# Performance work log

Hardware: AMD Instinct MI355X
Metric: run time of the kernel (lower is better)

## Reference

```python
import jax, jax.numpy as jnp
import numpy as np

B, L, E = 8, 2048, 128


def setup_inputs() -> dict:
    key = jax.random.key(0)
    k1, k2, k3, k4 = jax.random.split(key, 4)
    return {
        "Uq": jax.random.normal(k1, (B, L, E), dtype=jnp.float32),
        "Uid": jax.random.normal(k2, (B, L, E), dtype=jnp.float32),
        "mask": jnp.ones((L, L), dtype=jnp.float32),
        "Wc_w": jax.random.normal(k3, (3 * E,), dtype=jnp.float32) * 0.05,
        "Wc_b": jax.random.normal(k4, (), dtype=jnp.float32) * 0.05,
    }


def reference(Uq, Uid, mask, Wc_w, Wc_b):
    # Wc(cat(Uid, Uq, Uid*Uq)) decomposed into three direct projections —
    # exact same math as the Linear over the concatenation, never
    # materializing the [B, L, L, 3E] tensor.
    e = Uq.shape[-1]
    w_id, w_q, w_mul = Wc_w[:e], Wc_w[e:2 * e], Wc_w[2 * e:]
    s_id = jnp.einsum("bie,e->bi", Uid, w_id)          # [B, Lid]
    s_q = jnp.einsum("bje,e->bj", Uq, w_q)             # [B, Lq]
    s_mul = jnp.einsum("bie,bje,e->bij", Uid, Uq, w_mul)  # [B, Lid, Lq]
    S = (s_id[:, :, None] + s_q[:, None, :] + s_mul + Wc_b) * mask
    # S_D2Q = Softmax(dim=0) over the per-example [Lid, Lq] matrix -> axis=1
    P = jax.nn.softmax(S, axis=1)                      # [B, Lid, Lq]
    A_D2Q = jnp.einsum("bij,bje->bie", P, Uq)          # [B, Lid, E]
    M = jnp.einsum("bij,bkj->bik", P, P)               # P @ P^T, [B, Lid, Lid]
    A_Q2D = jnp.einsum("bik,bke->bie", M, Uid)         # [B, Lid, E]
    Vid = jnp.concatenate([Uid, A_D2Q, Uid * A_D2Q, Uid * A_Q2D], axis=-1)
    return Vid  # [B, Lid, 4E]
```

## Files before the change

kernel.cpp:

```cpp
#include <hip/hip_runtime.h>

#define L 2048
#define E 128
#define NB 8

typedef float f32x4 __attribute__((ext_vector_type(4)));
typedef short short8 __attribute__((ext_vector_type(8)));
typedef unsigned int u32;

static __device__ inline float bf2f(ushort u) {
  union { float f; u32 i; } v; v.i = ((u32)u) << 16; return v.f;
}
static __device__ inline ushort f2bf(float f) {
  union { float f; u32 i; } v; v.f = f;
  u32 x = v.i;
  return (ushort)((x + 0x7fffu + ((x >> 16) & 1u)) >> 16);
}

__device__ inline void glds16(const ushort* g, ushort* l) {
  __builtin_amdgcn_global_load_lds(
      (const __attribute__((address_space(1))) u32*)(const void*)g,
      (__attribute__((address_space(3))) u32*)(void*)l, 16, 0, 0);
}

__global__ __launch_bounds__(128) void k_prep(const float* __restrict__ Uq,
                                              const float* __restrict__ Uid,
                                              const float* __restrict__ Wcw,
                                              ushort* __restrict__ UqB,
                                              ushort* __restrict__ UidB,
                                              ushort* __restrict__ Uidw,
                                              float* __restrict__ s_id,
                                              float* __restrict__ s_q) {
  int r = blockIdx.x;
  int e = threadIdx.x;
  ushort uqu  = f2bf(Uq[(long)r * E + e]);
  ushort uidu = f2bf(Uid[(long)r * E + e]);
  float uqf = bf2f(uqu), uidf = bf2f(uidu);
  float wid  = bf2f(f2bf(Wcw[e]));
  float wq   = bf2f(f2bf(Wcw[E + e]));
  float wmul = bf2f(f2bf(Wcw[2 * E + e]));
  UqB[(long)r * E + e]  = uqu;
  UidB[(long)r * E + e] = uidu;
  Uidw[(long)r * E + e] = f2bf(uidf * wmul);
  float sid = uidf * wid, sq = uqf * wq;
  #pragma unroll
  for (int off = 32; off >= 1; off >>= 1) {
    sid += __shfl_down(sid, off, 64);
    sq  += __shfl_down(sq,  off, 64);
  }
  __shared__ float red[4];
  int wv = threadIdx.x >> 6;
  if ((threadIdx.x & 63) == 0) { red[wv * 2] = sid; red[wv * 2 + 1] = sq; }
  __syncthreads();
  if (threadIdx.x == 0) { s_id[r] = red[0] + red[2]; s_q[r] = red[1] + red[3]; }
}

__global__ __launch_bounds__(256) void k_maskT(const float* __restrict__ mask,
                                               ushort* __restrict__ maskT) {
  __shared__ ushort tile[32][33];
  int j0 = blockIdx.x * 32, i0 = blockIdx.y * 32;
  int tx = threadIdx.x, ty = threadIdx.y;
  #pragma unroll
  for (int r = ty; r < 32; r += 8)
    tile[r][tx] = f2bf(mask[(long)(i0 + r) * L + j0 + tx]);
  __syncthreads();
  #pragma unroll
  for (int r = ty; r < 32; r += 8)
    maskT[(long)(j0 + r) * L + i0 + tx] = tile[tx][r];
}

__global__ __launch_bounds__(256) void k_tr2(const ushort* __restrict__ s1,
                                             ushort* __restrict__ d1,
                                             const ushort* __restrict__ s2,
                                             ushort* __restrict__ d2) {
  __shared__ ushort tile[32][33];
  int zz = blockIdx.z;
  long base = (long)(zz & (NB - 1)) * L * E;
  const ushort* src = ((zz < NB) ? s1 : s2) + base;
  ushort* dst = ((zz < NB) ? d1 : d2) + base;
  int c0 = blockIdx.x * 32, r0 = blockIdx.y * 32;
  int tx = threadIdx.x, ty = threadIdx.y;
  #pragma unroll
  for (int i = ty; i < 32; i += 8)
    tile[i][tx] = src[(long)(r0 + i) * E + c0 + tx];
  __syncthreads();
  #pragma unroll
  for (int i = ty; i < 32; i += 8)
    dst[(long)(c0 + i) * L + r0 + tx] = tile[tx][i];
}

__device__ inline void gemm128_loop(const ushort* __restrict__ A,
                                    const ushort* __restrict__ B,
                                    long ldA, long ldB, int K,
                                    f32x4 acc[4][4],
                                    ushort* ldsA, ushort* ldsB) {
  const int t = threadIdx.x;
  const int w = t >> 6, lane = t & 63;
  const int mrow = lane & 15, quad = lane >> 4;
  const int lr = lane >> 3;
  const int lc = ((lane & 7) ^ lr) * 8;
  const int mh = (w & 1) * 64, nh = (w >> 1) * 64;
  for (int k0 = 0; k0 < K; k0 += 64) {
    __syncthreads();
    #pragma unroll
    for (int s = 0; s < 4; s++) {
      int row = w * 32 + s * 8 + lr;
      glds16(&A[(long)row * ldA + k0 + lc], &ldsA[w * 2048 + s * 512]);
      glds16(&B[(long)row * ldB + k0 + lc], &ldsB[w * 2048 + s * 512]);
    }
    __syncthreads();
    #pragma unroll
    for (int kk = 0; kk < 2; kk++) {
      short8 av[4], bv[4];
      #pragma unroll
      for (int mi = 0; mi < 4; mi++)
        av[mi] = *(const short8*)&ldsA[(mh + mi * 16 + mrow) * 64 +
                                       ((kk * 32 + quad * 8) ^ ((mrow & 7) << 3))];
      #pragma unroll
      for (int ni = 0; ni < 4; ni++)
        bv[ni] = *(const short8*)&ldsB[(nh + ni * 16 + mrow) * 64 +
                                       ((kk * 32 + quad * 8) ^ ((mrow & 7) << 3))];
      #pragma unroll
      for (int mi = 0; mi < 4; mi++)
        #pragma unroll
        for (int ni = 0; ni < 4; ni++)
          acc[mi][ni] = __builtin_amdgcn_mfma_f32_16x16x32_bf16(av[mi], bv[ni], acc[mi][ni], 0, 0, 0);
    }
  }
}

__device__ inline void gemm64x128_loop(const ushort* __restrict__ A,
                                       const ushort* __restrict__ B,
                                       long ldA, long ldB, int K,
                                       f32x4 acc[2][4],
                                       ushort* ldsA, ushort* ldsB) {
  const int t = threadIdx.x;
  const int w = t >> 6, lane = t & 63;
  const int mrow = lane & 15, quad = lane >> 4;
  const int lr = lane >> 3;
  const int lc = ((lane & 7) ^ lr) * 8;
  const int mh = (w & 1) * 32, nh = (w >> 1) * 64;
  for (int k0 = 0; k0 < K; k0 += 64) {
    __syncthreads();
    #pragma unroll
    for (int s = 0; s < 2; s++) {
      int row = w * 16 + s * 8 + lr;
      glds16(&A[(long)row * ldA + k0 + lc], &ldsA[w * 1024 + s * 512]);
    }
    #pragma unroll
    for (int s = 0; s < 4; s++) {
      int row = w * 32 + s * 8 + lr;
      glds16(&B[(long)row * ldB + k0 + lc], &ldsB[w * 2048 + s * 512]);
    }
    __syncthreads();
    #pragma unroll
    for (int kk = 0; kk < 2; kk++) {
      short8 av[2], bv[4];
      #pragma unroll
      for (int mi = 0; mi < 2; mi++)
        av[mi] = *(const short8*)&ldsA[(mh + mi * 16 + mrow) * 64 +
                                       ((kk * 32 + quad * 8) ^ ((mrow & 7) << 3))];
      #pragma unroll
      for (int ni = 0; ni < 4; ni++)
        bv[ni] = *(const short8*)&ldsB[(nh + ni * 16 + mrow) * 64 +
                                       ((kk * 32 + quad * 8) ^ ((mrow & 7) << 3))];
      #pragma unroll
      for (int mi = 0; mi < 2; mi++)
        #pragma unroll
        for (int ni = 0; ni < 4; ni++)
          acc[mi][ni] = __builtin_amdgcn_mfma_f32_16x16x32_bf16(av[mi], bv[ni], acc[mi][ni], 0, 0, 0);
    }
  }
}

__global__ __launch_bounds__(256) void k_scores(const ushort* __restrict__ Uq,
                                                const ushort* __restrict__ Uidw,
                                                const float* __restrict__ s_id,
                                                const float* __restrict__ s_q,
                                                const float* __restrict__ Wcb,
                                                const ushort* __restrict__ maskT,
                                                ushort* __restrict__ St,
                                                float* __restrict__ pm,
                                                float* __restrict__ ps, int b0) {
  __shared__ ushort lds[16384];
  ushort* ldsA = lds;
  ushort* ldsB = lds + 8192;
  int bz = blockIdx.z, b = b0 + bz;
  int m0 = blockIdx.x * 128;
  int n0 = blockIdx.y * 128;
  int tile_i = blockIdx.y;
  const ushort* A = Uq   + (long)b * L * E + (long)m0 * E;
  const ushort* B = Uidw + (long)b * L * E + (long)n0 * E;
  f32x4 acc[4][4] = {};
  gemm128_loop(A, B, E, E, E, acc, ldsA, ldsB);
  float bias = bf2f(f2bf(Wcb[0]));
  const int t = threadIdx.x, w = t >> 6, lane = t & 63;
  const int col = lane & 15, quad = lane >> 4;
  const int mh = (w & 1) * 64, nh = (w >> 1) * 64;

  __syncthreads();
  float sidv[4];
  #pragma unroll
  for (int ni = 0; ni < 4; ni++)
    sidv[ni] = s_id[b * L + n0 + nh + ni * 16 + col];
  #pragma unroll
  for (int mi = 0; mi < 4; mi++) {
    float sqv[4];
    #pragma unroll
    for (int rg = 0; rg < 4; rg++)
      sqv[rg] = s_q[b * L + m0 + mh + mi * 16 + quad * 4 + rg];
    #pragma unroll
    for (int ni = 0; ni < 4; ni++) {
      int cl = nh + ni * 16 + col;
      #pragma unroll
      for (int rg = 0; rg < 4; rg++) {
        int row = mh + mi * 16 + quad * 4 + rg;
        float v = acc[mi][ni][rg] + sqv[rg] + sidv[ni] + bias;
        lds[row * 128 + (cl ^ ((row & 7) << 3))] = f2bf(v);
      }
    }
  }
  __syncthreads();
  #pragma unroll
  for (int p = 0; p < 8; p++) {
    int r2 = p * 16 + (t >> 4);
    int cu = (t & 15) * 8;
    uint4 sv = *(const uint4*)&lds[r2 * 128 + (cu ^ ((r2 & 7) << 3))];
    int jg = m0 + r2;
    uint4 mv = *(const uint4*)&maskT[(long)jg * L + n0 + cu];
    ushort o[8]; float vv[8];
    const ushort* sp = (const ushort*)&sv;
    const ushort* mp = (const ushort*)&mv;
    #pragma unroll
    for (int k = 0; k < 8; k++) {
      o[k] = f2bf(bf2f(sp[k]) * bf2f(mp[k]));
      vv[k] = bf2f(o[k]);
    }
    *(uint4*)&St[(long)bz * L * L + (long)jg * L + n0 + cu] = *(const uint4*)&o[0];
    float lmx = vv[0];
    #pragma unroll
    for (int k = 1; k < 8; k++) lmx = fmaxf(lmx, vv[k]);
    #pragma unroll
    for (int off = 8; off >= 1; off >>= 1) lmx = fmaxf(lmx, __shfl_xor(lmx, off, 64));
    float lsum = 0.f;
    #pragma unroll
    for (int k = 0; k < 8; k++) lsum += __expf(vv[k] - lmx);
    #pragma unroll
    for (int off = 8; off >= 1; off >>= 1) lsum += __shfl_xor(lsum, off, 64);
    if ((t & 15) == 0) {
      long si = ((long)bz * L + jg) * 16 + tile_i;
      pm[si] = lmx; ps[si] = lsum;
    }
  }
}

__global__ __launch_bounds__(256) void k_sm_apply(ushort* __restrict__ St,
                                                  ushort* __restrict__ P,
                                                  const float* __restrict__ pm,
                                                  const float* __restrict__ ps) {
  __shared__ ushort tl[4 * 1056];
  __shared__ float smM[32], smI[32];
  int bz = blockIdx.y;
  int t = threadIdx.x, wid = t >> 6, lane = t & 63;
  int flat = blockIdx.x * 4 + wid;
  int j0 = (flat >> 6) * 32;
  int i0 = (flat & 63) * 32;
  if (t < 32) {
    const float* pmr = pm + ((long)bz * L + j0 + t) * 16;
    const float* psr = ps + ((long)bz * L + j0 + t) * 16;
    float m = pmr[0];
    #pragma unroll
    for (int k = 1; k < 16; k++) m = fmaxf(m, pmr[k]);
    float s = 0.f;
    #pragma unroll
    for (int k = 0; k < 16; k++) s += psr[k] * __expf(pmr[k] - m);
    smM[t] = m; smI[t] = 1.0f / s;
  }
  __syncthreads();
  ushort* Sb = St + (long)bz * L * L;
  ushort* Pb = P  + (long)bz * L * L;
  ushort* wt = tl + wid * 1056;
  int r = lane >> 1, c0 = (lane & 1) * 16;
  float m   = smM[r];
  float inv = smI[r];
  ushort* src = Sb + (long)(j0 + r) * L + i0 + c0;
  uint4 q0 = *(const uint4*)src;
  uint4 q1 = *(const uint4*)(src + 8);
  ushort o[16];
  const ushort* pr = (const ushort*)&q0;
  #pragma unroll
  for (int k = 0; k < 8; k++) o[k] = f2bf(__expf(bf2f(pr[k]) - m) * inv);
  pr = (const ushort*)&q1;
  #pragma unroll
  for (int k = 0; k < 8; k++) o[8 + k] = f2bf(__expf(bf2f(pr[k]) - m) * inv);
  *(uint4*)src       = *(const uint4*)&o[0];
  *(uint4*)(src + 8) = *(const uint4*)&o[8];
  #pragma unroll
  for (int k = 0; k < 16; k++) wt[(c0 + k) * 33 + r] = o[k];
  asm volatile("s_waitcnt lgkmcnt(0)" ::: "memory");
  __builtin_amdgcn_sched_barrier(0);
  ushort po[16];
  #pragma unroll
  for (int k = 0; k < 16; k++) po[k] = wt[r * 33 + c0 + k];
  ushort* pd = Pb + (long)(i0 + r) * L + j0 + c0;
  *(uint4*)pd       = *(const uint4*)&po[0];
  *(uint4*)(pd + 8) = *(const uint4*)&po[8];
}

__global__ __launch_bounds__(256) void k_gemm_Tt(const ushort* __restrict__ UidT,
                                                 const ushort* __restrict__ Pt,
                                                 ushort* __restrict__ Tt, int b0) {
  __shared__ ushort lds[12288];
  ushort* ldsA = lds;
  ushort* ldsB = lds + 4096;
  int bz = blockIdx.z, b = b0 + bz;
  int e0 = (blockIdx.x & 1) * 64;
  int j0 = (blockIdx.x >> 1) * 128;
  const ushort* A = UidT + (long)b * E * L + (long)e0 * L;
  const ushort* B = Pt   + (long)bz * L * L + (long)j0 * L;
  f32x4 acc[2][4] = {};
  gemm64x128_loop(A, B, L, L, L, acc, ldsA, ldsB);
  const int t = threadIdx.x, w = t >> 6, lane = t & 63;
  const int col = lane & 15, quad = lane >> 4;
  const int mh = (w & 1) * 32, nh = (w >> 1) * 64;
  __syncthreads();
  #pragma unroll
  for (int mi = 0; mi < 2; mi++)
    #pragma unroll
    for (int ni = 0; ni < 4; ni++) {
      int cl = nh + ni * 16 + col;
      #pragma unroll
      for (int rg = 0; rg < 4; rg++) {
        int row = mh + mi * 16 + quad * 4 + rg;
        lds[row * 128 + (cl ^ ((row & 7) << 3))] = f2bf(acc[mi][ni][rg]);
      }
    }
  __syncthreads();
  #pragma unroll
  for (int p = 0; p < 4; p++) {
    int r2 = p * 16 + (t >> 4);
    int cu = (t & 15) * 8;
    uint4 v = *(const uint4*)&lds[r2 * 128 + (cu ^ ((r2 & 7) << 3))];
    *(uint4*)&Tt[(long)b * E * L + (long)(e0 + r2) * L + j0 + cu] = v;
  }
}

__global__ __launch_bounds__(256) void k_gemm_A(const ushort* __restrict__ P,
                                                const ushort* __restrict__ UqT,
                                                const ushort* __restrict__ Tt,
                                                const ushort* __restrict__ UidB,
                                                float* __restrict__ out, int b0) {
  __shared__ ushort ldsA[64 * 64];
  __shared__ ushort ldsB[128 * 64];
  int bz = blockIdx.z, b = b0 + bz;
  int m0 = blockIdx.x * 64;
  int n0 = blockIdx.y * 128;
  const ushort* A = P + (long)bz * L * L + (long)m0 * L;
  const ushort* B = (blockIdx.y == 0) ? (UqT + (long)b * E * L)
                                      : (Tt  + (long)b * E * L);
  f32x4 acc[2][4] = {};
  gemm64x128_loop(A, B, L, L, L, acc, ldsA, ldsB);
  const int t = threadIdx.x, w = t >> 6, lane = t & 63;
  const int col = lane & 15, quad = lane >> 4;
  const int mh = (w & 1) * 32, nh = (w >> 1) * 64;
  #pragma unroll
  for (int mi = 0; mi < 2; mi++)
    #pragma unroll
    for (int ni = 0; ni < 4; ni++)
      #pragma unroll
      for (int rg = 0; rg < 4; rg++) {
        int ig = m0 + mh + mi * 16 + quad * 4 + rg;
        int c  = n0 + nh + ni * 16 + col;
        float a = acc[mi][ni][rg];
        float uidf = bf2f(UidB[(long)b * L * E + (long)ig * E + (c & 127)]);
        long ob = ((long)b * L + ig) * 512;
        if (c < 128) {
          out[ob + c]       = uidf;
          out[ob + 128 + c] = a;
          out[ob + 256 + c] = uidf * a;
        } else {
          out[ob + 256 + c] = uidf * a;
        }
      }
}

extern "C" void kernel_launch(void* const* d_in, const int* in_sizes, int n_in,
                              void* d_out, int out_size, void* d_ws, size_t ws_size,
                              hipStream_t stream) {
  const float* Uq   = (const float*)d_in[0];
  const float* Uid  = (const float*)d_in[1];
  const float* mask = (const float*)d_in[2];
  const float* Wcw  = (const float*)d_in[3];
  const float* Wcb  = (const float*)d_in[4];
  float* out = (float*)d_out;

  char* ws = (char*)d_ws;
  size_t off = 0;
  auto alloc = [&](size_t bytes) -> void* {
    void* p = ws + off; off += (bytes + 255) & ~(size_t)255; return p;
  };
  const size_t nUb = (size_t)NB * L * E * 2;
  ushort* UqB   = (ushort*)alloc(nUb);
  ushort* UidB  = (ushort*)alloc(nUb);
  ushort* Uidw  = (ushort*)alloc(nUb);
  ushort* UqT   = (ushort*)alloc(nUb);
  ushort* UidT  = (ushort*)alloc(nUb);
  ushort* Tt    = (ushort*)alloc(nUb);
  ushort* maskT = (ushort*)alloc((size_t)L * L * 2);
  float*  s_id  = (float*)alloc((size_t)NB * L * 4);
  float*  s_q   = (float*)alloc((size_t)NB * L * 4);
  float*  pm    = (float*)alloc((size_t)NB * L * 16 * 4);
  float*  ps    = (float*)alloc((size_t)NB * L * 16 * 4);
  const size_t per_batch = (size_t)L * L * 2;
  size_t avail = (ws_size > off + 2 * per_batch) ? (ws_size - off) : 2 * per_batch;
  int nb_c = (int)(avail / (2 * per_batch));
  if (nb_c < 1) nb_c = 1;
  if (nb_c > NB) nb_c = NB;
  ushort* St = (ushort*)(ws + off);
  ushort* P  = (ushort*)(ws + off + nb_c * per_batch);

  dim3 tb(32, 8);
  k_prep<<<NB * L, E, 0, stream>>>(Uq, Uid, Wcw, UqB, UidB, Uidw, s_id, s_q);
  k_maskT<<<dim3(L / 32, L / 32), tb, 0, stream>>>(mask, maskT);
  k_tr2<<<dim3(E / 32, L / 32, 2 * NB), tb, 0, stream>>>(UqB, UqT, UidB, UidT);

  for (int b0 = 0; b0 < NB; b0 += nb_c) {
    int nb = (NB - b0 < nb_c) ? (NB - b0) : nb_c;
    k_scores<<<dim3(L / 128, L / 128, nb), 256, 0, stream>>>(UqB, Uidw, s_id, s_q, Wcb, maskT, St, pm, ps, b0);
    k_sm_apply<<<dim3((L / 32) * (L / 32) / 4, nb), 256, 0, stream>>>(St, P, pm, ps);
    k_gemm_Tt<<<dim3(2 * (L / 128), 1, nb), 256, 0, stream>>>(UidT, St, Tt, b0);
    k_gemm_A<<<dim3(L / 64, 2, nb), 256, 0, stream>>>(P, UqT, Tt, UidB, out, b0);
  }
}
```

Baseline: 233.9 us.

## Drop softmax max-subtraction and defer normalization into GEMM epilogue

Scores kernel now writes exp(S) directly and emits only per-tile partial sums, removing the running max. A small kernel reduces the sums to a reciprocal per row. The transpose kernel only scales and transposes, no longer writing St back. The Tt GEMM consumes unnormalized exponentials and applies the reciprocal in its epilogue. This saves a full L×L read-modify-write pass and the exp work in the apply kernel, but risks overflow for large-magnitude scores because the max subtraction is gone.

```diff
diff --git a/kernel.cpp b/kernel.cpp
--- a/kernel.cpp
+++ b/kernel.cpp
@@ -180,7 +180,6 @@
                                                 const float* __restrict__ Wcb,
                                                 const ushort* __restrict__ maskT,
                                                 ushort* __restrict__ St,
-                                                float* __restrict__ pm,
                                                 float* __restrict__ ps, int b0) {
   __shared__ ushort lds[16384];
   ushort* ldsA = lds;
@@ -228,73 +227,59 @@
     uint4 sv = *(const uint4*)&lds[r2 * 128 + (cu ^ ((r2 & 7) << 3))];
     int jg = m0 + r2;
     uint4 mv = *(const uint4*)&maskT[(long)jg * L + n0 + cu];
-    ushort o[8]; float vv[8];
+    ushort o[8];
+    float lsum = 0.f;
     const ushort* sp = (const ushort*)&sv;
     const ushort* mp = (const ushort*)&mv;
     #pragma unroll
     for (int k = 0; k < 8; k++) {
-      o[k] = f2bf(bf2f(sp[k]) * bf2f(mp[k]));
-      vv[k] = bf2f(o[k]);
+      float ev = __expf(bf2f(sp[k]) * bf2f(mp[k]));
+      o[k] = f2bf(ev);
+      lsum += bf2f(o[k]);
     }
     *(uint4*)&St[(long)bz * L * L + (long)jg * L + n0 + cu] = *(const uint4*)&o[0];
-    float lmx = vv[0];
-    #pragma unroll
-    for (int k = 1; k < 8; k++) lmx = fmaxf(lmx, vv[k]);
-    #pragma unroll
-    for (int off = 8; off >= 1; off >>= 1) lmx = fmaxf(lmx, __shfl_xor(lmx, off, 64));
-    float lsum = 0.f;
-    #pragma unroll
-    for (int k = 0; k < 8; k++) lsum += __expf(vv[k] - lmx);
     #pragma unroll
     for (int off = 8; off >= 1; off >>= 1) lsum += __shfl_xor(lsum, off, 64);
     if ((t & 15) == 0) {
-      long si = ((long)bz * L + jg) * 16 + tile_i;
-      pm[si] = lmx; ps[si] = lsum;
-    }
-  }
-}
-
-__global__ __launch_bounds__(256) void k_sm_apply(ushort* __restrict__ St,
-                                                  ushort* __restrict__ P,
-                                                  const float* __restrict__ pm,
-                                                  const float* __restrict__ ps) {
+      ps[((long)bz * L + jg) * 16 + tile_i] = lsum;
+    }
+  }
+}
+
+__global__ __launch_bounds__(256) void k_redstats(const float* __restrict__ ps,
+                                                  float* __restrict__ lg) {
+  int idx = blockIdx.x * 256 + threadIdx.x;
+  const float* psr = ps + (long)idx * 16;
+  float s = 0.f;
+  #pragma unroll
+  for (int k = 0; k < 16; k++) s += psr[k];
+  lg[idx] = 1.0f / s;
+}
+
+__global__ __launch_bounds__(256) void k_ptr(const ushort* __restrict__ St,
+                                             ushort* __restrict__ P,
+                                             const float* __restrict__ lg) {
   __shared__ ushort tl[4 * 1056];
-  __shared__ float smM[32], smI[32];
   int bz = blockIdx.y;
   int t = threadIdx.x, wid = t >> 6, lane = t & 63;
   int flat = blockIdx.x * 4 + wid;
   int j0 = (flat >> 6) * 32;
   int i0 = (flat & 63) * 32;
-  if (t < 32) {
-    const float* pmr = pm + ((long)bz * L + j0 + t) * 16;
-    const float* psr = ps + ((long)bz * L + j0 + t) * 16;
-    float m = pmr[0];
-    #pragma unroll
-    for (int k = 1; k < 16; k++) m = fmaxf(m, pmr[k]);
-    float s = 0.f;
-    #pragma unroll
-    for (int k = 0; k < 16; k++) s += psr[k] * __expf(pmr[k] - m);
-    smM[t] = m; smI[t] = 1.0f / s;
-  }
-  __syncthreads();
-  ushort* Sb = St + (long)bz * L * L;
+  const ushort* Sb = St + (long)bz * L * L;
   ushort* Pb = P  + (long)bz * L * L;
   ushort* wt = tl + wid * 1056;
   int r = lane >> 1, c0 = (lane & 1) * 16;
-  float m   = smM[r];
-  float inv = smI[r];
-  ushort* src = Sb + (long)(j0 + r) * L + i0 + c0;
+  float inv = lg[bz * L + j0 + r];
+  const ushort* src = Sb + (long)(j0 + r) * L + i0 + c0;
   uint4 q0 = *(const uint4*)src;
   uint4 q1 = *(const uint4*)(src + 8);
   ushort o[16];
   const ushort* pr = (const ushort*)&q0;
   #pragma unroll
-  for (int k = 0; k < 8; k++) o[k] = f2bf(__expf(bf2f(pr[k]) - m) * inv);
+  for (int k = 0; k < 8; k++) o[k] = f2bf(bf2f(pr[k]) * inv);
   pr = (const ushort*)&q1;
   #pragma unroll
-  for (int k = 0; k < 8; k++) o[8 + k] = f2bf(__expf(bf2f(pr[k]) - m) * inv);
-  *(uint4*)src       = *(const uint4*)&o[0];
-  *(uint4*)(src + 8) = *(const uint4*)&o[8];
+  for (int k = 0; k < 8; k++) o[8 + k] = f2bf(bf2f(pr[k]) * inv);
   #pragma unroll
   for (int k = 0; k < 16; k++) wt[(c0 + k) * 33 + r] = o[k];
   asm volatile("s_waitcnt lgkmcnt(0)" ::: "memory");
@@ -308,7 +293,8 @@
 }
 
 __global__ __launch_bounds__(256) void k_gemm_Tt(const ushort* __restrict__ UidT,
-                                                 const ushort* __restrict__ Pt,
+                                                 const ushort* __restrict__ Et,
+                                                 const float* __restrict__ lg,
                                                  ushort* __restrict__ Tt, int b0) {
   __shared__ ushort lds[12288];
   ushort* ldsA = lds;
@@ -317,7 +303,7 @@
   int e0 = (blockIdx.x & 1) * 64;
   int j0 = (blockIdx.x >> 1) * 128;
   const ushort* A = UidT + (long)b * E * L + (long)e0 * L;
-  const ushort* B = Pt   + (long)bz * L * L + (long)j0 * L;
+  const ushort* B = Et   + (long)bz * L * L + (long)j0 * L;
   f32x4 acc[2][4] = {};
   gemm64x128_loop(A, B, L, L, L, acc, ldsA, ldsB);
   const int t = threadIdx.x, w = t >> 6, lane = t & 63;
@@ -329,10 +315,11 @@
     #pragma unroll
     for (int ni = 0; ni < 4; ni++) {
       int cl = nh + ni * 16 + col;
+      float sc = lg[(long)bz * L + j0 + cl];
       #pragma unroll
       for (int rg = 0; rg < 4; rg++) {
         int row = mh + mi * 16 + quad * 4 + rg;
-        lds[row * 128 + (cl ^ ((row & 7) << 3))] = f2bf(acc[mi][ni][rg]);
+        lds[row * 128 + (cl ^ ((row & 7) << 3))] = f2bf(acc[mi][ni][rg] * sc);
       }
     }
   __syncthreads();
@@ -409,7 +396,7 @@
   ushort* maskT = (ushort*)alloc((size_t)L * L * 2);
   float*  s_id  = (float*)alloc((size_t)NB * L * 4);
   float*  s_q   = (float*)alloc((size_t)NB * L * 4);
-  float*  pm    = (float*)alloc((size_t)NB * L * 16 * 4);
+  float*  lg    = (float*)alloc((size_t)NB * L * 4);
   float*  ps    = (float*)alloc((size_t)NB * L * 16 * 4);
   const size_t per_batch = (size_t)L * L * 2;
   size_t avail = (ws_size > off + 2 * per_batch) ? (ws_size - off) : 2 * per_batch;
@@ -426,9 +413,10 @@
 
   for (int b0 = 0; b0 < NB; b0 += nb_c) {
     int nb = (NB - b0 < nb_c) ? (NB - b0) : nb_c;
-    k_scores<<<dim3(L / 128, L / 128, nb), 256, 0, stream>>>(UqB, Uidw, s_id, s_q, Wcb, maskT, St, pm, ps, b0);
-    k_sm_apply<<<dim3((L / 32) * (L / 32) / 4, nb), 256, 0, stream>>>(St, P, pm, ps);
-    k_gemm_Tt<<<dim3(2 * (L / 128), 1, nb), 256, 0, stream>>>(UidT, St, Tt, b0);
+    k_scores<<<dim3(L / 128, L / 128, nb), 256, 0, stream>>>(UqB, Uidw, s_id, s_q, Wcb, maskT, St, ps, b0);
+    k_redstats<<<dim3(nb * L / 256), 256, 0, stream>>>(ps, lg);
+    k_ptr<<<dim3((L / 32) * (L / 32) / 4, nb), 256, 0, stream>>>(St, P, lg);
+    k_gemm_Tt<<<dim3(2 * (L / 128), 1, nb), 256, 0, stream>>>(UidT, St, lg, Tt, b0);
     k_gemm_A<<<dim3(L / 64, 2, nb), 256, 0, stream>>>(P, UqT, Tt, UidB, out, b0);
   }
 }
```

Result: faster. 224.5 us (-4.0%).
